# Performance work log

Hardware: AMD Instinct MI355X
Metric: run time of the kernel (lower is better)

The kernel has to match this reference:

```python
import jax, jax.numpy as jnp
import numpy as np

EPS = 1e-8  # matches torch F.cosine_similarity eps


def setup_inputs() -> dict:
    key = jax.random.key(0)
    k1, k2 = jax.random.split(key)
    num_nodes, feat_dim, num_edges = 100000, 128, 1600000
    node_features = jax.random.normal(k1, (num_nodes, feat_dim), dtype=jnp.float32)
    edge_index = jax.random.randint(k2, (2, num_edges), 0, num_nodes, dtype=jnp.int64)
    return {"node_features": node_features, "edge_index": edge_index}


def reference(node_features, edge_index):
    # Edge-parallel equivalent of the per-node loop:
    # each edge (s, d) contributes cos(u_s, u_d) to BOTH s and d
    # (the original adj dict appends both directions, duplicates included).
    num_nodes = node_features.shape[0]
    src, dst = edge_index[0], edge_index[1]

    # clamped norms as in torch cosine_similarity
    norms = jnp.maximum(jnp.linalg.norm(node_features, axis=-1), EPS)  # [N]

    # per-edge cosine similarity  [E]
    sim = jnp.einsum("ed,ed->e", node_features[src], node_features[dst]) / (
        norms[src] * norms[dst]
    )

    idx = jnp.concatenate([src, dst])            # [2E] — both endpoints
    vals = jnp.concatenate([sim, sim])           # [2E]
    sums = jax.ops.segment_sum(vals, idx, num_segments=num_nodes)          # [N]
    deg = jax.ops.segment_sum(jnp.ones_like(vals), idx, num_segments=num_nodes)

    # isolated nodes get similarity 1.0
    return jnp.where(deg > 0, sums / jnp.maximum(deg, 1.0), 1.0)
```

## Files before the change

### kernel.cpp

```cpp
#include <hip/hip_runtime.h>

#define FEAT 128
#define EPG 4
#define CNT_SHIFT 25
#define FIX_SCALE 32768.0f
#define INV_FIX (1.0f/32768.0f)
#define EPS 1e-8f

__device__ __forceinline__ unsigned xcc_id() {
    unsigned x;
    asm volatile("s_getreg_b32 %0, hwreg(HW_REG_XCC_ID)" : "=s"(x));
    return x & 7u;
}

__device__ __forceinline__ unsigned pack_sim(float sim) {
    return (1u << CNT_SHIFT) | (unsigned)((sim + 2.0f) * FIX_SCALE + 0.5f);
}

__device__ __forceinline__ int dot4(unsigned a, unsigned b, int c) {
#if __has_builtin(__builtin_amdgcn_sdot4)
    return __builtin_amdgcn_sdot4(a, b, c, false);
#else
    c += (int)(signed char)(a)        * (int)(signed char)(b);
    c += (int)(signed char)(a >> 8)   * (int)(signed char)(b >> 8);
    c += (int)(signed char)(a >> 16)  * (int)(signed char)(b >> 16);
    c += (int)(signed char)(a >> 24)  * (int)(signed char)(b >> 24);
    return c;
#endif
}

__device__ __forceinline__ int dot16(const uint4& a, const uint4& b) {
    int c = dot4(a.x, b.x, 0);
    c = dot4(a.y, b.y, c);
    c = dot4(a.z, b.z, c);
    return dot4(a.w, b.w, c);
}

__global__ void quantize_kernel(const float* __restrict__ feat,
                                unsigned short* __restrict__ tab16,
                                float* __restrict__ invq,
                                int num_nodes) {
    const int lane = threadIdx.x & 63;
    const int wpb = blockDim.x >> 6;
    int n = blockIdx.x * wpb + (threadIdx.x >> 6);
    const int stride = gridDim.x * wpb;
    for (; n < num_nodes; n += stride) {
        const float2 v = *reinterpret_cast<const float2*>(feat + (size_t)n * FEAT + lane * 2);
        float am = fmaxf(fabsf(v.x), fabsf(v.y));
        am = fmaxf(am, __shfl_xor(am, 32, 64));
        am = fmaxf(am, __shfl_xor(am, 16, 64));
        am = fmaxf(am, __shfl_xor(am, 8, 64));
        am = fmaxf(am, __shfl_xor(am, 4, 64));
        am = fmaxf(am, __shfl_xor(am, 2, 64));
        am = fmaxf(am, __shfl_xor(am, 1, 64));
        const float sc = (am > 0.0f) ? (127.0f / am) : 0.0f;
        const int qx = (int)rintf(v.x * sc);
        const int qy = (int)rintf(v.y * sc);
        int nq = qx * qx + qy * qy;
        nq += __shfl_xor(nq, 32, 64);
        nq += __shfl_xor(nq, 16, 64);
        nq += __shfl_xor(nq, 8, 64);
        nq += __shfl_xor(nq, 4, 64);
        nq += __shfl_xor(nq, 2, 64);
        nq += __shfl_xor(nq, 1, 64);
        tab16[(size_t)n * (FEAT / 2) + lane] =
            (unsigned short)((qx & 0xFF) | ((qy & 0xFF) << 8));
        if (lane == 0)
            invq[n] = (nq > 0) ? (1.0f / sqrtf((float)nq)) : 0.0f;
    }
}

template <int NCOPY>
__global__ void edge_i8_flat(const unsigned char* __restrict__ tab,
                             const int* __restrict__ ei,
                             const float* __restrict__ invq,
                             unsigned* __restrict__ acc,
                             int num_edges, int num_nodes, int aligned4) {
    unsigned* myacc = acc;
    if (NCOPY == 8) myacc = acc + (size_t)xcc_id() * num_nodes;

    const int sub = threadIdx.x & 7;
    const int gid = blockIdx.x * (blockDim.x >> 3) + (threadIdx.x >> 3);
    const int e0 = gid * EPG;
    if (e0 >= num_edges) return;

    int s[EPG], d[EPG];
    const bool fast = aligned4 && (e0 + EPG <= num_edges);
    if (fast) {
        const uint4 si = *reinterpret_cast<const uint4*>(ei + e0);
        const uint4 di = *reinterpret_cast<const uint4*>(ei + num_edges + e0);
        s[0] = (int)si.x; s[1] = (int)si.y; s[2] = (int)si.z; s[3] = (int)si.w;
        d[0] = (int)di.x; d[1] = (int)di.y; d[2] = (int)di.z; d[3] = (int)di.w;
    } else {
#pragma unroll
        for (int k = 0; k < EPG; ++k) {
            const int e = min(e0 + k, num_edges - 1);
            s[k] = ei[e];
            d[k] = ei[num_edges + e];
        }
    }

    uint4 a[EPG], b[EPG];
#pragma unroll
    for (int k = 0; k < EPG; ++k) {
        a[k] = reinterpret_cast<const uint4*>(tab + (size_t)s[k] * FEAT)[sub];
        b[k] = reinterpret_cast<const uint4*>(tab + (size_t)d[k] * FEAT)[sub];
    }

    int p[EPG];
#pragma unroll
    for (int k = 0; k < EPG; ++k) p[k] = dot16(a[k], b[k]);
#pragma unroll
    for (int k = 0; k < EPG; ++k) {
        p[k] += __shfl_xor(p[k], 1, 64);
        p[k] += __shfl_xor(p[k], 2, 64);
        p[k] += __shfl_xor(p[k], 4, 64);
    }

    int myidx = s[0];
    if (sub == 1) myidx = d[0];
    else if (sub == 2) myidx = s[1];
    else if (sub == 3) myidx = d[1];
    else if (sub == 4) myidx = s[2];
    else if (sub == 5) myidx = d[2];
    else if (sub == 6) myidx = s[3];
    else if (sub == 7) myidx = d[3];

    int mydot = p[0];
    if (sub >= 6) mydot = p[3];
    else if (sub >= 4) mydot = p[2];
    else if (sub >= 2) mydot = p[1];

    const float msc = invq[myidx];
    const float prod = msc * __shfl_xor(msc, 1, 64);

    if (fast || (e0 + (sub >> 1)) < num_edges) {
        const unsigned pk = pack_sim((float)mydot * prod);
        if (NCOPY == 8) {
            __hip_atomic_fetch_add(&myacc[myidx], pk, __ATOMIC_RELAXED,
                                   __HIP_MEMORY_SCOPE_WORKGROUP);
        } else {
            __hip_atomic_fetch_add(&myacc[myidx], pk, __ATOMIC_RELAXED,
                                   __HIP_MEMORY_SCOPE_AGENT);
        }
    }
}

__global__ void norms_inv_kernel(const float* __restrict__ feat,
                                 float* __restrict__ inv,
                                 int num_nodes) {
    const int lane = threadIdx.x & 63;
    const int wpb = blockDim.x >> 6;
    int n = blockIdx.x * wpb + (threadIdx.x >> 6);
    const int stride = gridDim.x * wpb;
    for (; n < num_nodes; n += stride) {
        const float2 v = *reinterpret_cast<const float2*>(feat + (size_t)n * FEAT + lane * 2);
        float s = v.x * v.x + v.y * v.y;
        s += __shfl_xor(s, 32, 64);
        s += __shfl_xor(s, 16, 64);
        s += __shfl_xor(s, 8, 64);
        s += __shfl_xor(s, 4, 64);
        s += __shfl_xor(s, 2, 64);
        s += __shfl_xor(s, 1, 64);
        if (lane == 0) inv[n] = 1.0f / fmaxf(sqrtf(s), EPS);
    }
}

__global__ void edge_f32_kernel(const float* __restrict__ feat,
                                const int* __restrict__ ei,
                                const float* __restrict__ inv,
                                unsigned* __restrict__ acc,
                                int num_edges) {
    const int sub = threadIdx.x & 31;
    const int gpb = blockDim.x >> 5;
    const int group = blockIdx.x * gpb + (threadIdx.x >> 5);
    const int ngroups = gridDim.x * gpb;
    for (int e = group; e < num_edges; e += ngroups) {
        const int s = ei[e];
        const int d = ei[num_edges + e];
        const float4 a = *reinterpret_cast<const float4*>(feat + (size_t)s * FEAT + sub * 4);
        const float4 b = *reinterpret_cast<const float4*>(feat + (size_t)d * FEAT + sub * 4);
        float p = a.x * b.x + a.y * b.y + a.z * b.z + a.w * b.w;
        p += __shfl_xor(p, 16, 64);
        p += __shfl_xor(p, 8, 64);
        p += __shfl_xor(p, 4, 64);
        p += __shfl_xor(p, 2, 64);
        p += __shfl_xor(p, 1, 64);
        const unsigned pk = pack_sim(p * inv[s] * inv[d]);
        if (sub == 0) atomicAdd(&acc[s], pk);
        else if (sub == 1) atomicAdd(&acc[d], pk);
    }
}

__global__ void final_kernel(const unsigned* __restrict__ acc,
                             float* __restrict__ out,
                             int num_nodes, int ncopies) {
    const int i = blockIdx.x * blockDim.x + threadIdx.x;
    if (i < num_nodes) {
        unsigned cnt = 0, fx = 0;
        for (int c = 0; c < ncopies; ++c) {
            const unsigned x = acc[(size_t)c * num_nodes + i];
            cnt += x >> CNT_SHIFT;
            fx += x & ((1u << CNT_SHIFT) - 1u);
        }
        out[i] = cnt ? ((float)fx * INV_FIX - 2.0f * (float)cnt) / (float)cnt : 1.0f;
    }
}

extern "C" void kernel_launch(void* const* d_in, const int* in_sizes, int n_in,
                              void* d_out, int out_size, void* d_ws, size_t ws_size,
                              hipStream_t stream) {
    const float* feat = (const float*)d_in[0];
    const int* ei = (const int*)d_in[1];
    const int num_nodes = in_sizes[0] / FEAT;
    const int num_edges = in_sizes[1] / 2;
    float* out = (float*)d_out;

    unsigned* acc = (unsigned*)d_ws;
    const size_t need8 = (size_t)num_nodes *
        (8 * sizeof(unsigned) + sizeof(float) + FEAT * sizeof(unsigned char));
    const size_t need1 = (size_t)num_nodes *
        (1 * sizeof(unsigned) + sizeof(float) + FEAT * sizeof(unsigned char));

    if (ws_size >= need1) {
        const int ncopy = (ws_size >= need8) ? 8 : 1;
        const size_t acc_bytes = (size_t)num_nodes * ncopy * sizeof(unsigned);
        float* invq = (float*)((char*)d_ws + acc_bytes);
        unsigned short* tab16 = (unsigned short*)(invq + num_nodes);
        hipMemsetAsync(acc, 0, acc_bytes, stream);
        {
            const int wpb = 4;
            int blocks = (num_nodes + wpb - 1) / wpb;
            if (blocks > 25000) blocks = 25000;
            quantize_kernel<<<blocks, 256, 0, stream>>>(feat, tab16, invq, num_nodes);
        }
        {
            const int epb = (256 / 8) * EPG;
            const int blocks = (num_edges + epb - 1) / epb;
            const int aligned4 = ((num_edges & 3) == 0) ? 1 : 0;
            if (ncopy == 8) {
                edge_i8_flat<8><<<blocks, 256, 0, stream>>>(
                    (const unsigned char*)tab16, ei, invq, acc,
                    num_edges, num_nodes, aligned4);
            } else {
                edge_i8_flat<1><<<blocks, 256, 0, stream>>>(
                    (const unsigned char*)tab16, ei, invq, acc,
                    num_edges, num_nodes, aligned4);
            }
        }
        final_kernel<<<(num_nodes + 255) / 256, 256, 0, stream>>>(acc, out, num_nodes, ncopy);
    } else {
        float* inv = (float*)((char*)d_ws + (size_t)num_nodes * sizeof(unsigned));
        hipMemsetAsync(acc, 0, (size_t)num_nodes * sizeof(unsigned), stream);
        {
            const int wpb = 4;
            int blocks = (num_nodes + wpb - 1) / wpb;
            norms_inv_kernel<<<blocks, 256, 0, stream>>>(feat, inv, num_nodes);
        }
        edge_f32_kernel<<<4096, 256, 0, stream>>>(feat, ei, inv, acc, num_edges);
        final_kernel<<<(num_nodes + 255) / 256, 256, 0, stream>>>(acc, out, num_nodes, 1);
    }
}
```

Before: 166.6 us.

## Replace global scatter atomics with per-edge sim buffer and LDS-chunked aggregation

The edge kernel no longer issues global atomics. It writes a 16-bit quantized similarity per edge to a workspace buffer. A new aggregation kernel then gives each block a node chunk of 16000 entries in LDS and an edge slice. The block rescans the edge indices and accumulates into LDS with shared-memory atomics, then writes a per-slice partial that the final kernel sums over up to 72 slices. This removes contended global atomic traffic and the memset, at the cost of re-reading the edge list once per chunk (7 chunks), extra sim buffer traffic, and coarser 16-bit quantization with a 24-bit count field.

```diff
diff --git a/kernel.cpp b/kernel.cpp
--- a/kernel.cpp
+++ b/kernel.cpp
@@ -2,20 +2,14 @@
 
 #define FEAT 128
 #define EPG 4
-#define CNT_SHIFT 25
-#define FIX_SCALE 32768.0f
-#define INV_FIX (1.0f/32768.0f)
+#define CHN 16000
+#define CNT_SHIFT 24
+#define SIM_SCALE 16384.0f
+#define INV_SIM (1.0f/16384.0f)
 #define EPS 1e-8f
 
-__device__ __forceinline__ unsigned xcc_id() {
-    unsigned x;
-    asm volatile("s_getreg_b32 %0, hwreg(HW_REG_XCC_ID)" : "=s"(x));
-    return x & 7u;
-}
-
-__device__ __forceinline__ unsigned pack_sim(float sim) {
-    return (1u << CNT_SHIFT) | (unsigned)((sim + 2.0f) * FIX_SCALE + 0.5f);
-}
+typedef unsigned uv4 __attribute__((ext_vector_type(4)));
+typedef unsigned short us4 __attribute__((ext_vector_type(4)));
 
 __device__ __forceinline__ int dot4(unsigned a, unsigned b, int c) {
 #if __has_builtin(__builtin_amdgcn_sdot4)
@@ -29,7 +23,7 @@
 #endif
 }
 
-__device__ __forceinline__ int dot16(const uint4& a, const uint4& b) {
+__device__ __forceinline__ int dot16(uv4 a, uv4 b) {
     int c = dot4(a.x, b.x, 0);
     c = dot4(a.y, b.y, c);
     c = dot4(a.z, b.z, c);
@@ -70,15 +64,11 @@
     }
 }
 
-template <int NCOPY>
-__global__ void edge_i8_flat(const unsigned char* __restrict__ tab,
-                             const int* __restrict__ ei,
-                             const float* __restrict__ invq,
-                             unsigned* __restrict__ acc,
-                             int num_edges, int num_nodes, int aligned4) {
-    unsigned* myacc = acc;
-    if (NCOPY == 8) myacc = acc + (size_t)xcc_id() * num_nodes;
-
+__global__ void edge_i8_sim(const unsigned char* __restrict__ tab,
+                            const int* __restrict__ ei,
+                            const float* __restrict__ invq,
+                            unsigned short* __restrict__ sim,
+                            int num_edges, int aligned4) {
     const int sub = threadIdx.x & 7;
     const int gid = blockIdx.x * (blockDim.x >> 3) + (threadIdx.x >> 3);
     const int e0 = gid * EPG;
@@ -87,8 +77,8 @@
     int s[EPG], d[EPG];
     const bool fast = aligned4 && (e0 + EPG <= num_edges);
     if (fast) {
-        const uint4 si = *reinterpret_cast<const uint4*>(ei + e0);
-        const uint4 di = *reinterpret_cast<const uint4*>(ei + num_edges + e0);
+        const uv4 si = *(const uv4*)(ei + e0);
+        const uv4 di = *(const uv4*)(ei + (size_t)num_edges + e0);
         s[0] = (int)si.x; s[1] = (int)si.y; s[2] = (int)si.z; s[3] = (int)si.w;
         d[0] = (int)di.x; d[1] = (int)di.y; d[2] = (int)di.z; d[3] = (int)di.w;
     } else {
@@ -96,15 +86,15 @@
         for (int k = 0; k < EPG; ++k) {
             const int e = min(e0 + k, num_edges - 1);
             s[k] = ei[e];
-            d[k] = ei[num_edges + e];
-        }
-    }
-
-    uint4 a[EPG], b[EPG];
+            d[k] = ei[(size_t)num_edges + e];
+        }
+    }
+
+    uv4 a[EPG], b[EPG];
 #pragma unroll
     for (int k = 0; k < EPG; ++k) {
-        a[k] = reinterpret_cast<const uint4*>(tab + (size_t)s[k] * FEAT)[sub];
-        b[k] = reinterpret_cast<const uint4*>(tab + (size_t)d[k] * FEAT)[sub];
+        a[k] = *(const uv4*)(tab + (size_t)s[k] * FEAT + sub * 16);
+        b[k] = *(const uv4*)(tab + (size_t)d[k] * FEAT + sub * 16);
     }
 
     int p[EPG];
@@ -126,84 +116,148 @@
     else if (sub == 6) myidx = s[3];
     else if (sub == 7) myidx = d[3];
 
+    const float msc = invq[myidx];
+    const float prod = msc * __shfl_xor(msc, 1, 64);
+
+    const int gb = (threadIdx.x & 63) & ~7;
+    const float pr0 = __shfl(prod, gb + 0, 64);
+    const float pr1 = __shfl(prod, gb + 2, 64);
+    const float pr2 = __shfl(prod, gb + 4, 64);
+    const float pr3 = __shfl(prod, gb + 6, 64);
+
+    if (sub == 0) {
+        us4 o;
+        o.x = (unsigned short)((float)p[0] * pr0 * SIM_SCALE + 32768.5f);
+        o.y = (unsigned short)((float)p[1] * pr1 * SIM_SCALE + 32768.5f);
+        o.z = (unsigned short)((float)p[2] * pr2 * SIM_SCALE + 32768.5f);
+        o.w = (unsigned short)((float)p[3] * pr3 * SIM_SCALE + 32768.5f);
+        *(us4*)(sim + e0) = o;
+    }
+}
+
+__global__ __launch_bounds__(1024)
+void agg_kernel(const int* __restrict__ ei,
+                const unsigned short* __restrict__ sim,
+                unsigned* __restrict__ acc,
+                int num_edges, int num_nodes, int CH, int S, int aligned4) {
+    __shared__ unsigned lds[CHN];
+    const int slice = blockIdx.x / CH;
+    const int chunk = blockIdx.x % CH;
+    const int base = chunk * CHN;
+    const int cn = min(CHN, num_nodes - base);
+
+    for (int i = threadIdx.x; i < cn; i += blockDim.x) lds[i] = 0;
+    __syncthreads();
+
+    const int P = (num_edges + 3) >> 2;
+    const int p0 = (int)((long long)P * slice / S);
+    const int p1 = (int)((long long)P * (slice + 1) / S);
+
+    for (int p = p0 + threadIdx.x; p < p1; p += blockDim.x) {
+        const int e0 = p * 4;
+        if (aligned4 && (e0 + 3 < num_edges)) {
+            const uv4 su = *(const uv4*)(ei + e0);
+            const uv4 du = *(const uv4*)(ei + (size_t)num_edges + e0);
+            const us4 sm = *(const us4*)(sim + e0);
+#pragma unroll
+            for (int k = 0; k < 4; ++k) {
+                const unsigned v = (1u << CNT_SHIFT) | (unsigned)sm[k];
+                const unsigned cs = (unsigned)((int)su[k] - base);
+                const unsigned cd = (unsigned)((int)du[k] - base);
+                if (cs < (unsigned)cn) atomicAdd(&lds[cs], v);
+                if (cd < (unsigned)cn) atomicAdd(&lds[cd], v);
+            }
+        } else {
+#pragma unroll
+            for (int k = 0; k < 4; ++k) {
+                const int e = e0 + k;
+                if (e < num_edges) {
+                    const unsigned v = (1u << CNT_SHIFT) | (unsigned)sim[e];
+                    const unsigned cs = (unsigned)(ei[e] - base);
+                    const unsigned cd = (unsigned)(ei[(size_t)num_edges + e] - base);
+                    if (cs < (unsigned)cn) atomicAdd(&lds[cs], v);
+                    if (cd < (unsigned)cn) atomicAdd(&lds[cd], v);
+                }
+            }
+        }
+    }
+    __syncthreads();
+    for (int i = threadIdx.x; i < cn; i += blockDim.x)
+        acc[(size_t)slice * num_nodes + base + i] = lds[i];
+}
+
+__global__ void edge_i8_atomic(const unsigned char* __restrict__ tab,
+                               const int* __restrict__ ei,
+                               const float* __restrict__ invq,
+                               unsigned* __restrict__ acc,
+                               int num_edges, int aligned4) {
+    const int sub = threadIdx.x & 7;
+    const int gid = blockIdx.x * (blockDim.x >> 3) + (threadIdx.x >> 3);
+    const int e0 = gid * EPG;
+    if (e0 >= num_edges) return;
+    int s[EPG], d[EPG];
+    const bool fast = aligned4 && (e0 + EPG <= num_edges);
+    if (fast) {
+        const uv4 si = *(const uv4*)(ei + e0);
+        const uv4 di = *(const uv4*)(ei + (size_t)num_edges + e0);
+        s[0] = (int)si.x; s[1] = (int)si.y; s[2] = (int)si.z; s[3] = (int)si.w;
+        d[0] = (int)di.x; d[1] = (int)di.y; d[2] = (int)di.z; d[3] = (int)di.w;
+    } else {
+#pragma unroll
+        for (int k = 0; k < EPG; ++k) {
+            const int e = min(e0 + k, num_edges - 1);
+            s[k] = ei[e];
+            d[k] = ei[(size_t)num_edges + e];
+        }
+    }
+    uv4 a[EPG], b[EPG];
+#pragma unroll
+    for (int k = 0; k < EPG; ++k) {
+        a[k] = *(const uv4*)(tab + (size_t)s[k] * FEAT + sub * 16);
+        b[k] = *(const uv4*)(tab + (size_t)d[k] * FEAT + sub * 16);
+    }
+    int p[EPG];
+#pragma unroll
+    for (int k = 0; k < EPG; ++k) p[k] = dot16(a[k], b[k]);
+#pragma unroll
+    for (int k = 0; k < EPG; ++k) {
+        p[k] += __shfl_xor(p[k], 1, 64);
+        p[k] += __shfl_xor(p[k], 2, 64);
+        p[k] += __shfl_xor(p[k], 4, 64);
+    }
+    int myidx = s[0];
+    if (sub == 1) myidx = d[0];
+    else if (sub == 2) myidx = s[1];
+    else if (sub == 3) myidx = d[1];
+    else if (sub == 4) myidx = s[2];
+    else if (sub == 5) myidx = d[2];
+    else if (sub == 6) myidx = s[3];
+    else if (sub == 7) myidx = d[3];
     int mydot = p[0];
     if (sub >= 6) mydot = p[3];
     else if (sub >= 4) mydot = p[2];
     else if (sub >= 2) mydot = p[1];
-
     const float msc = invq[myidx];
     const float prod = msc * __shfl_xor(msc, 1, 64);
-
     if (fast || (e0 + (sub >> 1)) < num_edges) {
-        const unsigned pk = pack_sim((float)mydot * prod);
-        if (NCOPY == 8) {
-            __hip_atomic_fetch_add(&myacc[myidx], pk, __ATOMIC_RELAXED,
-                                   __HIP_MEMORY_SCOPE_WORKGROUP);
-        } else {
-            __hip_atomic_fetch_add(&myacc[myidx], pk, __ATOMIC_RELAXED,
-                                   __HIP_MEMORY_SCOPE_AGENT);
-        }
-    }
-}
-
-__global__ void norms_inv_kernel(const float* __restrict__ feat,
-                                 float* __restrict__ inv,
-                                 int num_nodes) {
-    const int lane = threadIdx.x & 63;
-    const int wpb = blockDim.x >> 6;
-    int n = blockIdx.x * wpb + (threadIdx.x >> 6);
-    const int stride = gridDim.x * wpb;
-    for (; n < num_nodes; n += stride) {
-        const float2 v = *reinterpret_cast<const float2*>(feat + (size_t)n * FEAT + lane * 2);
-        float s = v.x * v.x + v.y * v.y;
-        s += __shfl_xor(s, 32, 64);
-        s += __shfl_xor(s, 16, 64);
-        s += __shfl_xor(s, 8, 64);
-        s += __shfl_xor(s, 4, 64);
-        s += __shfl_xor(s, 2, 64);
-        s += __shfl_xor(s, 1, 64);
-        if (lane == 0) inv[n] = 1.0f / fmaxf(sqrtf(s), EPS);
-    }
-}
-
-__global__ void edge_f32_kernel(const float* __restrict__ feat,
-                                const int* __restrict__ ei,
-                                const float* __restrict__ inv,
-                                unsigned* __restrict__ acc,
-                                int num_edges) {
-    const int sub = threadIdx.x & 31;
-    const int gpb = blockDim.x >> 5;
-    const int group = blockIdx.x * gpb + (threadIdx.x >> 5);
-    const int ngroups = gridDim.x * gpb;
-    for (int e = group; e < num_edges; e += ngroups) {
-        const int s = ei[e];
-        const int d = ei[num_edges + e];
-        const float4 a = *reinterpret_cast<const float4*>(feat + (size_t)s * FEAT + sub * 4);
-        const float4 b = *reinterpret_cast<const float4*>(feat + (size_t)d * FEAT + sub * 4);
-        float p = a.x * b.x + a.y * b.y + a.z * b.z + a.w * b.w;
-        p += __shfl_xor(p, 16, 64);
-        p += __shfl_xor(p, 8, 64);
-        p += __shfl_xor(p, 4, 64);
-        p += __shfl_xor(p, 2, 64);
-        p += __shfl_xor(p, 1, 64);
-        const unsigned pk = pack_sim(p * inv[s] * inv[d]);
-        if (sub == 0) atomicAdd(&acc[s], pk);
-        else if (sub == 1) atomicAdd(&acc[d], pk);
+        const unsigned pk = (1u << CNT_SHIFT) |
+            (unsigned)((float)mydot * prod * SIM_SCALE + 32768.5f);
+        atomicAdd(&acc[myidx], pk);
     }
 }
 
 __global__ void final_kernel(const unsigned* __restrict__ acc,
                              float* __restrict__ out,
-                             int num_nodes, int ncopies) {
+                             int num_nodes, int S) {
     const int i = blockIdx.x * blockDim.x + threadIdx.x;
     if (i < num_nodes) {
         unsigned cnt = 0, fx = 0;
-        for (int c = 0; c < ncopies; ++c) {
+        for (int c = 0; c < S; ++c) {
             const unsigned x = acc[(size_t)c * num_nodes + i];
             cnt += x >> CNT_SHIFT;
             fx += x & ((1u << CNT_SHIFT) - 1u);
         }
-        out[i] = cnt ? ((float)fx * INV_FIX - 2.0f * (float)cnt) / (float)cnt : 1.0f;
+        out[i] = cnt ? ((float)fx * INV_SIM - 2.0f * (float)cnt) / (float)cnt : 1.0f;
     }
 }
 
@@ -215,49 +269,51 @@
     const int num_nodes = in_sizes[0] / FEAT;
     const int num_edges = in_sizes[1] / 2;
     float* out = (float*)d_out;
-
-    unsigned* acc = (unsigned*)d_ws;
-    const size_t need8 = (size_t)num_nodes *
-        (8 * sizeof(unsigned) + sizeof(float) + FEAT * sizeof(unsigned char));
-    const size_t need1 = (size_t)num_nodes *
-        (1 * sizeof(unsigned) + sizeof(float) + FEAT * sizeof(unsigned char));
-
-    if (ws_size >= need1) {
-        const int ncopy = (ws_size >= need8) ? 8 : 1;
-        const size_t acc_bytes = (size_t)num_nodes * ncopy * sizeof(unsigned);
-        float* invq = (float*)((char*)d_ws + acc_bytes);
-        unsigned short* tab16 = (unsigned short*)(invq + num_nodes);
-        hipMemsetAsync(acc, 0, acc_bytes, stream);
-        {
-            const int wpb = 4;
-            int blocks = (num_nodes + wpb - 1) / wpb;
-            if (blocks > 25000) blocks = 25000;
-            quantize_kernel<<<blocks, 256, 0, stream>>>(feat, tab16, invq, num_nodes);
-        }
+    const int aligned4 = ((num_edges & 3) == 0) ? 1 : 0;
+
+    const size_t padE = (size_t)((num_edges + 3) & ~3) + 4;
+    const size_t off_invq = padE * sizeof(unsigned short);
+    const size_t off_tab = off_invq + (size_t)num_nodes * sizeof(float);
+    const size_t off_acc = off_tab + (size_t)num_nodes * FEAT;
+
+    unsigned short* sim = (unsigned short*)d_ws;
+    float* invq = (float*)((char*)d_ws + off_invq);
+    unsigned short* tab16 = (unsigned short*)((char*)d_ws + off_tab);
+    unsigned* acc = (unsigned*)((char*)d_ws + off_acc);
+
+    int S = 0;
+    if (ws_size > off_acc) {
+        const size_t avail = ws_size - off_acc;
+        size_t smax = avail / ((size_t)num_nodes * sizeof(unsigned));
+        S = (int)((smax > 72) ? 72 : smax);
+    }
+    const int CH = (num_nodes + CHN - 1) / CHN;
+
+    {
+        const int wpb = 4;
+        int blocks = (num_nodes + wpb - 1) / wpb;
+        if (blocks > 25000) blocks = 25000;
+        quantize_kernel<<<blocks, 256, 0, stream>>>(feat, tab16, invq, num_nodes);
+    }
+
+    if (S >= 8 && aligned4) {
         {
             const int epb = (256 / 8) * EPG;
             const int blocks = (num_edges + epb - 1) / epb;
-            const int aligned4 = ((num_edges & 3) == 0) ? 1 : 0;
-            if (ncopy == 8) {
-                edge_i8_flat<8><<<blocks, 256, 0, stream>>>(
-                    (const unsigned char*)tab16, ei, invq, acc,
-                    num_edges, num_nodes, aligned4);
-            } else {
-                edge_i8_flat<1><<<blocks, 256, 0, stream>>>(
-                    (const unsigned char*)tab16, ei, invq, acc,
-                    num_edges, num_nodes, aligned4);
-            }
-        }
-        final_kernel<<<(num_nodes + 255) / 256, 256, 0, stream>>>(acc, out, num_nodes, ncopy);
+            edge_i8_sim<<<blocks, 256, 0, stream>>>(
+                (const unsigned char*)tab16, ei, invq, sim, num_edges, aligned4);
+        }
+        agg_kernel<<<CH * S, 1024, 0, stream>>>(ei, sim, acc, num_edges,
+                                                num_nodes, CH, S, aligned4);
+        final_kernel<<<(num_nodes + 255) / 256, 256, 0, stream>>>(acc, out, num_nodes, S);
     } else {
-        float* inv = (float*)((char*)d_ws + (size_t)num_nodes * sizeof(unsigned));
         hipMemsetAsync(acc, 0, (size_t)num_nodes * sizeof(unsigned), stream);
         {
-            const int wpb = 4;
-            int blocks = (num_nodes + wpb - 1) / wpb;
-            norms_inv_kernel<<<blocks, 256, 0, stream>>>(feat, inv, num_nodes);
-        }
-        edge_f32_kernel<<<4096, 256, 0, stream>>>(feat, ei, inv, acc, num_edges);
+            const int epb = (256 / 8) * EPG;
+            const int blocks = (num_edges + epb - 1) / epb;
+            edge_i8_atomic<<<blocks, 256, 0, stream>>>(
+                (const unsigned char*)tab16, ei, invq, acc, num_edges, aligned4);
+        }
         final_kernel<<<(num_nodes + 255) / 256, 256, 0, stream>>>(acc, out, num_nodes, 1);
     }
 }
```

New measurement: 151.7 us. -8.9%, faster.
